# Optimization experiments

Hardware: AMD Instinct MI355X
Metric: run time of the kernel (lower is better)

## Reference

```python
import jax, jax.numpy as jnp
import numpy as np

N_NODES = 100000
N_EDGES = 3200000
NODE_F = 256
EDGE_F = 16
N_HEAD = 8
OUT_F = 256
NEG_SLOPE = 0.2
BN_EPS = 1e-5


def _seg_softmax(e, idx, num_segments):
    # numerically stable segment softmax over edges grouped by idx
    m = jax.ops.segment_max(e, idx, num_segments=num_segments)
    ex = jnp.exp(e - m[idx])
    s = jax.ops.segment_sum(ex, idx, num_segments=num_segments)
    return ex / s[idx]


def setup_inputs() -> dict:
    key = jax.random.key(0)
    ks = jax.random.split(key, 16)
    inp = {}
    inp["feat_src"] = jax.random.normal(ks[0], (N_NODES, NODE_F), jnp.float32)
    inp["feat_edge"] = jax.random.normal(ks[1], (N_EDGES, EDGE_F), jnp.float32)
    inp["src"] = jax.random.randint(ks[2], (N_EDGES,), 0, N_NODES, jnp.int32)
    inp["dst"] = jax.random.randint(ks[3], (N_EDGES,), 0, N_NODES, jnp.int32)
    def xav(k, fan_in, fan_out):
        # xavier_normal with relu gain sqrt(2)
        std = np.sqrt(2.0) * np.sqrt(2.0 / (fan_in + fan_out))
        return jax.random.normal(k, (fan_in, fan_out), jnp.float32) * std
    inp["W_prop_src"] = xav(ks[4], NODE_F, N_HEAD)
    inp["W_attn_src"] = xav(ks[5], NODE_F, N_HEAD)
    inp["W_attn_dst"] = xav(ks[6], NODE_F, N_HEAD)
    inp["W_attn_edge"] = xav(ks[7], EDGE_F, N_HEAD)
    inp["bn_gamma"] = jnp.ones((N_HEAD,), jnp.float32)
    inp["bn_beta"] = jnp.zeros((N_HEAD,), jnp.float32)
    inp["W_agg"] = xav(ks[8], N_HEAD, OUT_F)
    inp["b_agg"] = jnp.zeros((OUT_F,), jnp.float32)
    inp["W_apply_dst"] = xav(ks[9], NODE_F, OUT_F)
    inp["b_apply_dst"] = jnp.zeros((OUT_F,), jnp.float32)
    inp["W_apply"] = xav(ks[10], OUT_F, OUT_F)
    inp["b_apply"] = jnp.zeros((OUT_F,), jnp.float32)
    return inp


def reference(feat_src, feat_edge, src, dst, W_prop_src, W_attn_src, W_attn_dst,
              W_attn_edge, bn_gamma, bn_beta, W_agg, b_agg, W_apply_dst,
              b_apply_dst, W_apply, b_apply):
    leaky = lambda x: jnp.where(x >= 0, x, NEG_SLOPE * x)
    feat_dst = feat_src  # non-block graph
    feat_src_fc = feat_src @ W_prop_src            # [N, H]
    attn_src = feat_src @ W_attn_src               # [N, H]
    attn_dst = feat_dst @ W_attn_dst               # [N, H]
    attn_edge = feat_edge @ W_attn_edge            # [E, H]
    e = attn_src[src] + attn_dst[dst] + attn_edge  # [E, H]
    e = leaky(e)                                   # edge_att_actv = leaky_relu
    # dual softmax: geometric mean of dst- and src-normalized softmaxes
    a_dst = jnp.clip(_seg_softmax(e, dst, N_NODES), 1e-9)
    a_src = jnp.clip(_seg_softmax(e, src, N_NODES), 1e-9)
    a = jnp.sqrt(a_dst * a_src)                    # [E, H]
    msg_sum = jax.ops.segment_sum(feat_src_fc[src] * a, dst, num_segments=N_NODES)  # [N, H]
    # BatchNorm1d (training mode: batch statistics over nodes, biased var)
    mu = jnp.mean(msg_sum, axis=0)
    var = jnp.mean((msg_sum - mu) ** 2, axis=0)
    h = (msg_sum - mu) / jnp.sqrt(var + BN_EPS) * bn_gamma + bn_beta
    rst = h @ W_agg + b_agg                        # [N, OUT]
    rst = rst + feat_dst @ W_apply_dst + b_apply_dst
    rst = leaky(rst)
    rst = rst @ W_apply + b_apply
    return rst
```

## Files before the change

kernel.cpp:

```cpp
#include <hip/hip_runtime.h>

#define LRELU(x) ((x) >= 0.0f ? (x) : 0.2f * (x))

typedef __attribute__((ext_vector_type(8))) short short8;
typedef __attribute__((ext_vector_type(4))) float f32x4;

__device__ __forceinline__ unsigned short f2bf(float f) {
    union { float f; unsigned int u; } v; v.f = f;
    unsigned int u = v.u;
    u += 0x7FFFu + ((u >> 16) & 1u);
    return (unsigned short)(u >> 16);
}

__global__ __launch_bounds__(256) void k_node_tables(
    const float* __restrict__ feat,
    const float* __restrict__ Wp, const float* __restrict__ Was,
    const float* __restrict__ Wad,
    float* __restrict__ fc, float* __restrict__ as_t, float* __restrict__ ad_t,
    int N)
{
    __shared__ float Wl[3 * 2048];
    for (int i = threadIdx.x; i < 3 * 2048; i += 256) {
        float v;
        if (i < 2048)      v = Wp[i];
        else if (i < 4096) v = Was[i - 2048];
        else               v = Wad[i - 4096];
        Wl[i] = v;
    }
    __syncthreads();
    int gid = blockIdx.x * 256 + threadIdx.x;
    int n = gid >> 3, h = gid & 7;
    if (n >= N) return;
    const float4* f4 = (const float4*)(feat + (size_t)n * 256);
    float aP = 0.f, aS = 0.f, aD = 0.f;
#pragma unroll 8
    for (int k4 = 0; k4 < 64; ++k4) {
        float4 f = f4[k4];
        int b = k4 * 32 + h;
        aP += f.x * Wl[b]        + f.y * Wl[b + 8]        + f.z * Wl[b + 16]        + f.w * Wl[b + 24];
        aS += f.x * Wl[2048 + b] + f.y * Wl[2048 + b + 8] + f.z * Wl[2048 + b + 16] + f.w * Wl[2048 + b + 24];
        aD += f.x * Wl[4096 + b] + f.y * Wl[4096 + b + 8] + f.z * Wl[4096 + b + 16] + f.w * Wl[4096 + b + 24];
    }
    fc[gid] = aP; as_t[gid] = aS; ad_t[gid] = aD;
}

__device__ __forceinline__ float edge_ex(
    const float* __restrict__ feat_edge, const float* Wl,
    const float* __restrict__ as_t, const float* __restrict__ ad_t,
    int e, int h, int s, int d)
{
    const float4* fe = (const float4*)(feat_edge + (size_t)e * 16);
    float4 f0 = fe[0], f1 = fe[1], f2 = fe[2], f3 = fe[3];
    float ae = f0.x * Wl[h]      + f0.y * Wl[h + 8]   + f0.z * Wl[h + 16]  + f0.w * Wl[h + 24]
             + f1.x * Wl[h + 32] + f1.y * Wl[h + 40]  + f1.z * Wl[h + 48]  + f1.w * Wl[h + 56]
             + f2.x * Wl[h + 64] + f2.y * Wl[h + 72]  + f2.z * Wl[h + 80]  + f2.w * Wl[h + 88]
             + f3.x * Wl[h + 96] + f3.y * Wl[h + 104] + f3.z * Wl[h + 112] + f3.w * Wl[h + 120];
    float ev = as_t[s * 8 + h] + ad_t[d * 8 + h] + ae;
    ev = LRELU(ev);
    return __expf(ev);
}

__global__ __launch_bounds__(256) void k_edge1(
    const float* __restrict__ feat_edge,
    const int* __restrict__ src, const int* __restrict__ dst,
    const float* __restrict__ We,
    const float* __restrict__ as_t, const float* __restrict__ ad_t,
    float* __restrict__ sum_dst, float* __restrict__ sum_src, int E)
{
    __shared__ float Wl[128];
    if (threadIdx.x < 128) Wl[threadIdx.x] = We[threadIdx.x];
    __syncthreads();
    int gid = blockIdx.x * 256 + threadIdx.x;
    int e = gid >> 3, h = gid & 7;
    if (e >= E) return;
    int s = src[e], d = dst[e];
    float ex = edge_ex(feat_edge, Wl, as_t, ad_t, e, h, s, d);
    atomicAdd(&sum_dst[d * 8 + h], ex);
    atomicAdd(&sum_src[s * 8 + h], ex);
}

__global__ __launch_bounds__(256) void k_edge2(
    const float* __restrict__ feat_edge,
    const int* __restrict__ src, const int* __restrict__ dst,
    const float* __restrict__ We,
    const float* __restrict__ as_t, const float* __restrict__ ad_t,
    const float* __restrict__ sum_dst, const float* __restrict__ sum_src,
    const float* __restrict__ fc, float* __restrict__ msg, int E)
{
    __shared__ float Wl[128];
    if (threadIdx.x < 128) Wl[threadIdx.x] = We[threadIdx.x];
    __syncthreads();
    int gid = blockIdx.x * 256 + threadIdx.x;
    int e = gid >> 3, h = gid & 7;
    if (e >= E) return;
    int s = src[e], d = dst[e];
    float ex = edge_ex(feat_edge, Wl, as_t, ad_t, e, h, s, d);
    float a_d = fmaxf(ex / sum_dst[d * 8 + h], 1e-9f);
    float a_s = fmaxf(ex / sum_src[s * 8 + h], 1e-9f);
    float a = sqrtf(a_d * a_s);
    atomicAdd(&msg[d * 8 + h], fc[s * 8 + h] * a);
}

__global__ __launch_bounds__(256) void k_bn_stats(
    const float* __restrict__ msg, float* __restrict__ accum, int N)
{
    __shared__ float s1[8], s2[8];
    if (threadIdx.x < 8) { s1[threadIdx.x] = 0.f; s2[threadIdx.x] = 0.f; }
    __syncthreads();
    int h = threadIdx.x & 7;
    float a1 = 0.f, a2 = 0.f;
    int total = N * 8;
    for (int i = blockIdx.x * 256 + threadIdx.x; i < total; i += gridDim.x * 256) {
        float x = msg[i];
        a1 += x; a2 += x * x;
    }
    atomicAdd(&s1[h], a1);
    atomicAdd(&s2[h], a2);
    __syncthreads();
    if (threadIdx.x < 8) {
        atomicAdd(&accum[threadIdx.x], s1[threadIdx.x]);
        atomicAdd(&accum[8 + threadIdx.x], s2[threadIdx.x]);
    }
}

__global__ __launch_bounds__(256) void k_bn_apply(
    const float* __restrict__ msg, const float* __restrict__ accum,
    const float* __restrict__ gamma, const float* __restrict__ beta,
    float* __restrict__ h_t, int N)
{
    int i = blockIdx.x * 256 + threadIdx.x;
    if (i >= N * 8) return;
    int h = i & 7;
    float invN = 1.0f / (float)N;
    float mu = accum[h] * invN;
    float var = accum[8 + h] * invN - mu * mu;
    float rstd = rsqrtf(var + 1e-5f);
    h_t[i] = (msg[i] - mu) * rstd * gamma[h] + beta[h];
}

__global__ __launch_bounds__(256) void k_prep(
    const float* __restrict__ W1, const float* __restrict__ Wagg,
    const float* __restrict__ W2,
    const float* __restrict__ b_agg, const float* __restrict__ b1,
    const float* __restrict__ b2,
    unsigned short* __restrict__ B1t, unsigned short* __restrict__ B2t,
    float* __restrict__ bias1, float* __restrict__ bias2)
{
    int idx = blockIdx.x * 256 + threadIdx.x;
    if (idx < 73728) {
        int c = idx >> 13, rem = idx & 8191;
        int n = rem >> 5, k = rem & 31;
        float v;
        if (c < 8) v = W1[(c * 32 + k) * 256 + n];
        else       v = (k < 8) ? Wagg[k * 256 + n] : 0.f;
        B1t[idx] = f2bf(v);
    } else if (idx < 139264) {
        int j = idx - 73728;
        int c = j >> 13, rem = j & 8191;
        int n = rem >> 5, k = rem & 31;
        B2t[j] = f2bf(W2[(c * 32 + k) * 256 + n]);
    } else if (idx < 139520) {
        int n = idx - 139264;
        bias1[n] = b_agg[n] + b1[n];
    } else if (idx < 139776) {
        int n = idx - 139520;
        bias2[n] = b2[n];
    }
}

#define ASTRIDE 296

__global__ __launch_bounds__(256, 2) void k_fused_apply(
    const float* __restrict__ feat, const float* __restrict__ h_t,
    const unsigned short* __restrict__ B1t,
    const unsigned short* __restrict__ B2t,
    const float* __restrict__ bias1, const float* __restrict__ bias2,
    float* __restrict__ out, int N)
{
    __shared__ __align__(16) unsigned short As[64 * ASTRIDE];
    __shared__ __align__(16) unsigned short Bs[8192];

    int tid = threadIdx.x;
    int row0 = blockIdx.x * 64;

#pragma unroll
    for (int t = 0; t < 16; ++t) {
        int i = tid + t * 256;
        int r = i >> 6, k4 = i & 63;
        float4 f = make_float4(0.f, 0.f, 0.f, 0.f);
        if (row0 + r < N)
            f = ((const float4*)(feat + (size_t)(row0 + r) * 256))[k4];
        ushort4 b;
        b.x = f2bf(f.x); b.y = f2bf(f.y); b.z = f2bf(f.z); b.w = f2bf(f.w);
        *(ushort4*)&As[r * ASTRIDE + k4 * 4] = b;
    }
#pragma unroll
    for (int t = 0; t < 8; ++t) {
        int e = tid + t * 256;
        int r = e >> 5, c = e & 31;
        float v = 0.f;
        if (c < 8 && row0 + r < N) v = h_t[(size_t)(row0 + r) * 8 + c];
        As[r * ASTRIDE + 256 + c] = f2bf(v);
    }

    int wave = tid >> 6;
    int lane = tid & 63;
    int n16  = lane & 15;
    int quad = lane >> 4;
    int col0 = wave * 64;

    f32x4 acc[4][4];
#pragma unroll
    for (int rt = 0; rt < 4; ++rt)
#pragma unroll
        for (int ct = 0; ct < 4; ++ct)
            acc[rt][ct] = (f32x4){0.f, 0.f, 0.f, 0.f};

    for (int kc = 0; kc < 9; ++kc) {
        __syncthreads();
#pragma unroll
        for (int t = 0; t < 4; ++t) {
            int i = tid + t * 256;
            ((float4*)Bs)[i] = ((const float4*)(B1t + kc * 8192))[i];
        }
        __syncthreads();
        int kbase = kc * 32;
        short8 af[4], bf[4];
#pragma unroll
        for (int rt = 0; rt < 4; ++rt)
            af[rt] = *(const short8*)&As[(rt * 16 + n16) * ASTRIDE + kbase + quad * 8];
#pragma unroll
        for (int ct = 0; ct < 4; ++ct)
            bf[ct] = *(const short8*)&Bs[(col0 + ct * 16 + n16) * 32 + quad * 8];
#pragma unroll
        for (int rt = 0; rt < 4; ++rt)
#pragma unroll
            for (int ct = 0; ct < 4; ++ct)
                acc[rt][ct] = __builtin_amdgcn_mfma_f32_16x16x32_bf16(
                    af[rt], bf[ct], acc[rt][ct], 0, 0, 0);
    }

    float bi[4];
#pragma unroll
    for (int ct = 0; ct < 4; ++ct) bi[ct] = bias1[col0 + ct * 16 + n16];
    __syncthreads();
#pragma unroll
    for (int rt = 0; rt < 4; ++rt)
#pragma unroll
        for (int ct = 0; ct < 4; ++ct)
#pragma unroll
            for (int r = 0; r < 4; ++r) {
                float v = acc[rt][ct][r] + bi[ct];
                v = LRELU(v);
                int row = rt * 16 + quad * 4 + r;
                int col = col0 + ct * 16 + n16;
                As[row * ASTRIDE + col] = f2bf(v);
            }

#pragma unroll
    for (int rt = 0; rt < 4; ++rt)
#pragma unroll
        for (int ct = 0; ct < 4; ++ct)
            acc[rt][ct] = (f32x4){0.f, 0.f, 0.f, 0.f};

    for (int kc = 0; kc < 8; ++kc) {
        __syncthreads();
#pragma unroll
        for (int t = 0; t < 4; ++t) {
            int i = tid + t * 256;
            ((float4*)Bs)[i] = ((const float4*)(B2t + kc * 8192))[i];
        }
        __syncthreads();
        int kbase = kc * 32;
        short8 af[4], bf[4];
#pragma unroll
        for (int rt = 0; rt < 4; ++rt)
            af[rt] = *(const short8*)&As[(rt * 16 + n16) * ASTRIDE + kbase + quad * 8];
#pragma unroll
        for (int ct = 0; ct < 4; ++ct)
            bf[ct] = *(const short8*)&Bs[(col0 + ct * 16 + n16) * 32 + quad * 8];
#pragma unroll
        for (int rt = 0; rt < 4; ++rt)
#pragma unroll
            for (int ct = 0; ct < 4; ++ct)
                acc[rt][ct] = __builtin_amdgcn_mfma_f32_16x16x32_bf16(
                    af[rt], bf[ct], acc[rt][ct], 0, 0, 0);
    }

    float bi2[4];
#pragma unroll
    for (int ct = 0; ct < 4; ++ct) bi2[ct] = bias2[col0 + ct * 16 + n16];
#pragma unroll
    for (int rt = 0; rt < 4; ++rt)
#pragma unroll
        for (int r = 0; r < 4; ++r) {
            int row = row0 + rt * 16 + quad * 4 + r;
            if (row < N) {
#pragma unroll
                for (int ct = 0; ct < 4; ++ct) {
                    int col = col0 + ct * 16 + n16;
                    out[(size_t)row * 256 + col] = acc[rt][ct][r] + bi2[ct];
                }
            }
        }
}

extern "C" void kernel_launch(void* const* d_in, const int* in_sizes, int n_in,
                              void* d_out, int out_size, void* d_ws, size_t ws_size,
                              hipStream_t stream)
{
    const float* feat      = (const float*)d_in[0];
    const float* feat_edge = (const float*)d_in[1];
    const int*   src       = (const int*)d_in[2];
    const int*   dst       = (const int*)d_in[3];
    const float* W_prop    = (const float*)d_in[4];
    const float* W_as      = (const float*)d_in[5];
    const float* W_ad      = (const float*)d_in[6];
    const float* W_edge    = (const float*)d_in[7];
    const float* bn_gamma  = (const float*)d_in[8];
    const float* bn_beta   = (const float*)d_in[9];
    const float* W_agg     = (const float*)d_in[10];
    const float* b_agg     = (const float*)d_in[11];
    const float* W1        = (const float*)d_in[12];
    const float* b1        = (const float*)d_in[13];
    const float* W2        = (const float*)d_in[14];
    const float* b2        = (const float*)d_in[15];
    float* out = (float*)d_out;

    int N = in_sizes[0] / 256;
    int E = in_sizes[2];
    int N8 = N * 8;

    float* ws       = (float*)d_ws;
    float* sum_dst  = ws;
    float* sum_src  = sum_dst + N8;
    float* msg      = sum_src + N8;
    float* accum    = msg + N8;
    float* fc       = accum + 16;
    float* as_t     = fc + N8;
    float* ad_t     = as_t + N8;
    float* h_t      = ad_t + N8;
    float* bias1    = h_t + N8;
    float* bias2    = bias1 + 256;
    unsigned short* B1t = (unsigned short*)(bias2 + 256);
    unsigned short* B2t = B1t + 73728;

    hipMemsetAsync(d_ws, 0, (size_t)(3 * N8 + 16) * sizeof(float), stream);

    int gridN8 = (N8 + 255) / 256;
    int gridE8 = (E * 8 + 255) / 256;
    int gridF  = (N + 63) / 64;

    k_prep<<<546, 256, 0, stream>>>(W1, W_agg, W2, b_agg, b1, b2,
                                    B1t, B2t, bias1, bias2);
    k_node_tables<<<gridN8, 256, 0, stream>>>(feat, W_prop, W_as, W_ad,
                                              fc, as_t, ad_t, N);
    k_edge1<<<gridE8, 256, 0, stream>>>(feat_edge, src, dst, W_edge,
                                        as_t, ad_t, sum_dst, sum_src, E);
    k_edge2<<<gridE8, 256, 0, stream>>>(feat_edge, src, dst, W_edge,
                                        as_t, ad_t, sum_dst, sum_src,
                                        fc, msg, E);
    k_bn_stats<<<512, 256, 0, stream>>>(msg, accum, N);
    k_bn_apply<<<gridN8, 256, 0, stream>>>(msg, accum, bn_gamma, bn_beta, h_t, N);
    k_fused_apply<<<gridF, 256, 0, stream>>>(feat, h_t, B1t, B2t,
                                             bias1, bias2, out, N);
}
```

Measured before the change: 1.068 ms.

## Replace edge atomics with CSR build and per-node segmented reductions

The two atomic-heavy edge passes are replaced by a CSR construction per call (histogram, two-level scan, atomic scatter of edge ids) for both dst and src. Edge exp values are computed once per edge across all 8 heads and stored in a buffer. Per-node wavefront kernels then gather these to form the src sums and the dst-normalized messages without float atomics. This removes the recomputation and the float atomic contention, but adds several kernel launches, integer atomics in the histogram and scatter, a 100 MB exp buffer, and random gathers through edge-id indirection.

```diff
diff --git a/kernel.cpp b/kernel.cpp
--- a/kernel.cpp
+++ b/kernel.cpp
@@ -44,61 +44,193 @@
     fc[gid] = aP; as_t[gid] = aS; ad_t[gid] = aD;
 }
 
-__device__ __forceinline__ float edge_ex(
-    const float* __restrict__ feat_edge, const float* Wl,
-    const float* __restrict__ as_t, const float* __restrict__ ad_t,
-    int e, int h, int s, int d)
-{
-    const float4* fe = (const float4*)(feat_edge + (size_t)e * 16);
-    float4 f0 = fe[0], f1 = fe[1], f2 = fe[2], f3 = fe[3];
-    float ae = f0.x * Wl[h]      + f0.y * Wl[h + 8]   + f0.z * Wl[h + 16]  + f0.w * Wl[h + 24]
-             + f1.x * Wl[h + 32] + f1.y * Wl[h + 40]  + f1.z * Wl[h + 48]  + f1.w * Wl[h + 56]
-             + f2.x * Wl[h + 64] + f2.y * Wl[h + 72]  + f2.z * Wl[h + 80]  + f2.w * Wl[h + 88]
-             + f3.x * Wl[h + 96] + f3.y * Wl[h + 104] + f3.z * Wl[h + 112] + f3.w * Wl[h + 120];
-    float ev = as_t[s * 8 + h] + ad_t[d * 8 + h] + ae;
-    ev = LRELU(ev);
-    return __expf(ev);
-}
-
-__global__ __launch_bounds__(256) void k_edge1(
+__global__ __launch_bounds__(256) void k_hist(
+    const int* __restrict__ src, const int* __restrict__ dst,
+    int* __restrict__ cnt_dst, int* __restrict__ cnt_src, int E)
+{
+    int e = blockIdx.x * 256 + threadIdx.x;
+    if (e >= E) return;
+    atomicAdd(&cnt_dst[dst[e]], 1);
+    atomicAdd(&cnt_src[src[e]], 1);
+}
+
+__global__ __launch_bounds__(256) void k_scan_blk(
+    const int* __restrict__ cnt_dst, const int* __restrict__ cnt_src,
+    int* __restrict__ bsum, int N, int nblk)
+{
+    int b = blockIdx.x;
+    const int* cnt = (b < nblk) ? cnt_dst : cnt_src;
+    int bb = (b < nblk) ? b : b - nblk;
+    int i = bb * 256 + threadIdx.x;
+    int v = (i < N) ? cnt[i] : 0;
+    __shared__ int ls[4];
+    for (int m = 1; m < 64; m <<= 1) v += __shfl_xor(v, m);
+    if ((threadIdx.x & 63) == 0) ls[threadIdx.x >> 6] = v;
+    __syncthreads();
+    if (threadIdx.x == 0) bsum[b] = ls[0] + ls[1] + ls[2] + ls[3];
+}
+
+__global__ __launch_bounds__(1024) void k_scan_top(
+    const int* __restrict__ bsum, int* __restrict__ bscan, int nblk)
+{
+    __shared__ int s[1024];
+    int t = threadIdx.x;
+    int li = t & 511;
+    int seg = t >> 9;
+    int v = (li < nblk) ? bsum[seg * nblk + li] : 0;
+    s[t] = v;
+    __syncthreads();
+    for (int d = 1; d < 512; d <<= 1) {
+        int add = (li >= d) ? s[t - d] : 0;
+        __syncthreads();
+        s[t] += add;
+        __syncthreads();
+    }
+    if (li < nblk) bscan[seg * nblk + li] = s[t] - v;
+}
+
+__global__ __launch_bounds__(256) void k_scan_fin(
+    const int* __restrict__ cnt_dst, const int* __restrict__ cnt_src,
+    const int* __restrict__ bscan,
+    int* __restrict__ start_dst, int* __restrict__ start_src,
+    int* __restrict__ cur_dst, int* __restrict__ cur_src, int N, int nblk)
+{
+    __shared__ int s[256];
+    int b = blockIdx.x;
+    bool isdst = (b < nblk);
+    const int* cnt = isdst ? cnt_dst : cnt_src;
+    int bb = isdst ? b : b - nblk;
+    int i = bb * 256 + threadIdx.x;
+    int t = threadIdx.x;
+    int v = (i < N) ? cnt[i] : 0;
+    s[t] = v;
+    __syncthreads();
+    for (int d = 1; d < 256; d <<= 1) {
+        int add = (t >= d) ? s[t - d] : 0;
+        __syncthreads();
+        s[t] += add;
+        __syncthreads();
+    }
+    int st = s[t] - v + bscan[b];
+    if (i < N) {
+        if (isdst) { start_dst[i] = st; cur_dst[i] = st; }
+        else       { start_src[i] = st; cur_src[i] = st; }
+    }
+}
+
+__global__ __launch_bounds__(256) void k_scatter(
+    const int* __restrict__ src, const int* __restrict__ dst,
+    int* __restrict__ cur_dst, int* __restrict__ cur_src,
+    int* __restrict__ eid_dst, int* __restrict__ eid_src, int E)
+{
+    int e = blockIdx.x * 256 + threadIdx.x;
+    if (e >= E) return;
+    int p = atomicAdd(&cur_dst[dst[e]], 1);
+    eid_dst[p] = e;
+    int q = atomicAdd(&cur_src[src[e]], 1);
+    eid_src[q] = e;
+}
+
+__global__ __launch_bounds__(256) void k_edge_ex(
     const float* __restrict__ feat_edge,
     const int* __restrict__ src, const int* __restrict__ dst,
     const float* __restrict__ We,
     const float* __restrict__ as_t, const float* __restrict__ ad_t,
-    float* __restrict__ sum_dst, float* __restrict__ sum_src, int E)
+    float* __restrict__ ex_buf, int E)
 {
     __shared__ float Wl[128];
     if (threadIdx.x < 128) Wl[threadIdx.x] = We[threadIdx.x];
     __syncthreads();
-    int gid = blockIdx.x * 256 + threadIdx.x;
-    int e = gid >> 3, h = gid & 7;
+    int e = blockIdx.x * 256 + threadIdx.x;
     if (e >= E) return;
     int s = src[e], d = dst[e];
-    float ex = edge_ex(feat_edge, Wl, as_t, ad_t, e, h, s, d);
-    atomicAdd(&sum_dst[d * 8 + h], ex);
-    atomicAdd(&sum_src[s * 8 + h], ex);
-}
-
-__global__ __launch_bounds__(256) void k_edge2(
-    const float* __restrict__ feat_edge,
-    const int* __restrict__ src, const int* __restrict__ dst,
-    const float* __restrict__ We,
-    const float* __restrict__ as_t, const float* __restrict__ ad_t,
-    const float* __restrict__ sum_dst, const float* __restrict__ sum_src,
-    const float* __restrict__ fc, float* __restrict__ msg, int E)
-{
-    __shared__ float Wl[128];
-    if (threadIdx.x < 128) Wl[threadIdx.x] = We[threadIdx.x];
-    __syncthreads();
-    int gid = blockIdx.x * 256 + threadIdx.x;
-    int e = gid >> 3, h = gid & 7;
-    if (e >= E) return;
-    int s = src[e], d = dst[e];
-    float ex = edge_ex(feat_edge, Wl, as_t, ad_t, e, h, s, d);
-    float a_d = fmaxf(ex / sum_dst[d * 8 + h], 1e-9f);
-    float a_s = fmaxf(ex / sum_src[s * 8 + h], 1e-9f);
-    float a = sqrtf(a_d * a_s);
-    atomicAdd(&msg[d * 8 + h], fc[s * 8 + h] * a);
+    const float4* fe = (const float4*)(feat_edge + (size_t)e * 16);
+    float4 f0 = fe[0], f1 = fe[1], f2 = fe[2], f3 = fe[3];
+    float4 sa = *(const float4*)(as_t + (size_t)s * 8);
+    float4 sb = *(const float4*)(as_t + (size_t)s * 8 + 4);
+    float4 da = *(const float4*)(ad_t + (size_t)d * 8);
+    float4 db = *(const float4*)(ad_t + (size_t)d * 8 + 4);
+    float sv[8] = {sa.x, sa.y, sa.z, sa.w, sb.x, sb.y, sb.z, sb.w};
+    float dv[8] = {da.x, da.y, da.z, da.w, db.x, db.y, db.z, db.w};
+    float exo[8];
+#pragma unroll
+    for (int h = 0; h < 8; ++h) {
+        float ae = f0.x * Wl[h]      + f0.y * Wl[h + 8]   + f0.z * Wl[h + 16]  + f0.w * Wl[h + 24]
+                 + f1.x * Wl[h + 32] + f1.y * Wl[h + 40]  + f1.z * Wl[h + 48]  + f1.w * Wl[h + 56]
+                 + f2.x * Wl[h + 64] + f2.y * Wl[h + 72]  + f2.z * Wl[h + 80]  + f2.w * Wl[h + 88]
+                 + f3.x * Wl[h + 96] + f3.y * Wl[h + 104] + f3.z * Wl[h + 112] + f3.w * Wl[h + 120];
+        float ev = sv[h] + dv[h] + ae;
+        ev = LRELU(ev);
+        exo[h] = __expf(ev);
+    }
+    float4* o = (float4*)(ex_buf + (size_t)e * 8);
+    o[0] = make_float4(exo[0], exo[1], exo[2], exo[3]);
+    o[1] = make_float4(exo[4], exo[5], exo[6], exo[7]);
+}
+
+__global__ __launch_bounds__(256) void k_sum_src(
+    const int* __restrict__ start_src, const int* __restrict__ cnt_src,
+    const int* __restrict__ eid_src, const float* __restrict__ ex_buf,
+    float* __restrict__ sum_src, int N)
+{
+    int w = (blockIdx.x * 256 + threadIdx.x) >> 6;
+    if (w >= N) return;
+    int lane = threadIdx.x & 63;
+    int h = lane & 7, j0 = lane >> 3;
+    int st = start_src[w], deg = cnt_src[w];
+    float acc = 0.f;
+    for (int base = 0; base < deg; base += 8) {
+        int idx = base + j0;
+        if (idx < deg) {
+            int eid = eid_src[st + idx];
+            acc += ex_buf[(size_t)eid * 8 + h];
+        }
+    }
+    acc += __shfl_xor(acc, 8);
+    acc += __shfl_xor(acc, 16);
+    acc += __shfl_xor(acc, 32);
+    if (lane < 8) sum_src[(size_t)w * 8 + lane] = acc;
+}
+
+__global__ __launch_bounds__(256) void k_dst_msg(
+    const int* __restrict__ start_dst, const int* __restrict__ cnt_dst,
+    const int* __restrict__ eid_dst, const int* __restrict__ src,
+    const float* __restrict__ ex_buf, const float* __restrict__ sum_src,
+    const float* __restrict__ fc, float* __restrict__ msg, int N)
+{
+    int w = (blockIdx.x * 256 + threadIdx.x) >> 6;
+    if (w >= N) return;
+    int lane = threadIdx.x & 63;
+    int h = lane & 7, j0 = lane >> 3;
+    int st = start_dst[w], deg = cnt_dst[w];
+    float sd = 0.f;
+    for (int base = 0; base < deg; base += 8) {
+        int idx = base + j0;
+        if (idx < deg)
+            sd += ex_buf[(size_t)eid_dst[st + idx] * 8 + h];
+    }
+    sd += __shfl_xor(sd, 8);
+    sd += __shfl_xor(sd, 16);
+    sd += __shfl_xor(sd, 32);
+    float inv_sd = 1.0f / sd;
+    float macc = 0.f;
+    for (int base = 0; base < deg; base += 8) {
+        int idx = base + j0;
+        if (idx < deg) {
+            int eid = eid_dst[st + idx];
+            float ex = ex_buf[(size_t)eid * 8 + h];
+            int s = src[eid];
+            float ss = sum_src[(size_t)s * 8 + h];
+            float fcv = fc[(size_t)s * 8 + h];
+            float a_d = fmaxf(ex * inv_sd, 1e-9f);
+            float a_s = fmaxf(ex / ss, 1e-9f);
+            macc += fcv * sqrtf(a_d * a_s);
+        }
+    }
+    macc += __shfl_xor(macc, 8);
+    macc += __shfl_xor(macc, 16);
+    macc += __shfl_xor(macc, 32);
+    if (lane < 8) msg[(size_t)w * 8 + lane] = macc;
 }
 
 __global__ __launch_bounds__(256) void k_bn_stats(
@@ -330,36 +462,57 @@
     int N = in_sizes[0] / 256;
     int E = in_sizes[2];
     int N8 = N * 8;
+    int nblk = (N + 255) / 256;
 
     float* ws       = (float*)d_ws;
-    float* sum_dst  = ws;
-    float* sum_src  = sum_dst + N8;
+    float* accum    = ws;
+    int*   cnt_dst  = (int*)(accum + 16);
+    int*   cnt_src  = cnt_dst + N;
+    float* sum_src  = (float*)(cnt_src + N);
     float* msg      = sum_src + N8;
-    float* accum    = msg + N8;
-    float* fc       = accum + 16;
+    float* fc       = msg + N8;
     float* as_t     = fc + N8;
     float* ad_t     = as_t + N8;
     float* h_t      = ad_t + N8;
     float* bias1    = h_t + N8;
     float* bias2    = bias1 + 256;
-    unsigned short* B1t = (unsigned short*)(bias2 + 256);
+    int*   start_dst= (int*)(bias2 + 256);
+    int*   start_src= start_dst + N;
+    int*   cur_dst  = start_src + N;
+    int*   cur_src  = cur_dst + N;
+    int*   bsum     = cur_src + N;
+    int*   bscan    = bsum + 1024;
+    int*   eid_dst  = bscan + 1024;
+    int*   eid_src  = eid_dst + E;
+    unsigned short* B1t = (unsigned short*)(eid_src + E);
     unsigned short* B2t = B1t + 73728;
-
-    hipMemsetAsync(d_ws, 0, (size_t)(3 * N8 + 16) * sizeof(float), stream);
+    float* ex_buf   = (float*)(B2t + 65536);
+
+    hipMemsetAsync(d_ws, 0, (size_t)(16 + 2 * N) * sizeof(float), stream);
 
     int gridN8 = (N8 + 255) / 256;
-    int gridE8 = (E * 8 + 255) / 256;
+    int gridE  = (E + 255) / 256;
+    int gridW  = (N + 3) / 4;
     int gridF  = (N + 63) / 64;
 
     k_prep<<<546, 256, 0, stream>>>(W1, W_agg, W2, b_agg, b1, b2,
                                     B1t, B2t, bias1, bias2);
     k_node_tables<<<gridN8, 256, 0, stream>>>(feat, W_prop, W_as, W_ad,
                                               fc, as_t, ad_t, N);
-    k_edge1<<<gridE8, 256, 0, stream>>>(feat_edge, src, dst, W_edge,
-                                        as_t, ad_t, sum_dst, sum_src, E);
-    k_edge2<<<gridE8, 256, 0, stream>>>(feat_edge, src, dst, W_edge,
-                                        as_t, ad_t, sum_dst, sum_src,
-                                        fc, msg, E);
+    k_hist<<<gridE, 256, 0, stream>>>(src, dst, cnt_dst, cnt_src, E);
+    k_scan_blk<<<2 * nblk, 256, 0, stream>>>(cnt_dst, cnt_src, bsum, N, nblk);
+    k_scan_top<<<1, 1024, 0, stream>>>(bsum, bscan, nblk);
+    k_scan_fin<<<2 * nblk, 256, 0, stream>>>(cnt_dst, cnt_src, bscan,
+                                             start_dst, start_src,
+                                             cur_dst, cur_src, N, nblk);
+    k_scatter<<<gridE, 256, 0, stream>>>(src, dst, cur_dst, cur_src,
+                                         eid_dst, eid_src, E);
+    k_edge_ex<<<gridE, 256, 0, stream>>>(feat_edge, src, dst, W_edge,
+                                         as_t, ad_t, ex_buf, E);
+    k_sum_src<<<gridW, 256, 0, stream>>>(start_src, cnt_src, eid_src,
+                                         ex_buf, sum_src, N);
+    k_dst_msg<<<gridW, 256, 0, stream>>>(start_dst, cnt_dst, eid_dst, src,
+                                         ex_buf, sum_src, fc, msg, N);
     k_bn_stats<<<512, 256, 0, stream>>>(msg, accum, N);
     k_bn_apply<<<gridN8, 256, 0, stream>>>(msg, accum, bn_gamma, bn_beta, h_t, N);
     k_fused_apply<<<gridF, 256, 0, stream>>>(feat, h_t, B1t, B2t,
```

New measurement: 1.808 ms. +69.4%, slower.
